# Optimization experiments

Measured on AMD Instinct MI355X. Metric: run time of the kernel, lower is better.

Reference implementation:

```python
import jax, jax.numpy as jnp
import numpy as np

D_MODEL = 512
KEY_DIM = 512
VALUE_DIM = 512
N_HEADS = 8


def setup_inputs() -> dict:
    key = jax.random.key(0)
    ks = jax.random.split(key, 12)
    B, S = 8, 1024
    s = 0.02
    return {
        "input1": jax.random.normal(ks[0], (B, S, D_MODEL), jnp.float32),
        "input2": jax.random.normal(ks[1], (B, S, D_MODEL), jnp.float32),
        "input3": jax.random.normal(ks[2], (B, S, D_MODEL), jnp.float32),
        # per-head projection weights stacked over heads: [H, D, d]
        "Wq": jax.random.normal(ks[3], (N_HEADS, D_MODEL, KEY_DIM), jnp.float32) * s,
        "bq": jnp.zeros((N_HEADS, KEY_DIM), jnp.float32),
        "Wk": jax.random.normal(ks[4], (N_HEADS, D_MODEL, KEY_DIM), jnp.float32) * s,
        "bk": jnp.zeros((N_HEADS, KEY_DIM), jnp.float32),
        "Wv": jax.random.normal(ks[5], (N_HEADS, D_MODEL, VALUE_DIM), jnp.float32) * s,
        "bv": jnp.zeros((N_HEADS, VALUE_DIM), jnp.float32),
        # output projection: concat of heads (H*VALUE_DIM) -> KEY_DIM
        "Wo": jax.random.normal(ks[6], (N_HEADS * VALUE_DIM, KEY_DIM), jnp.float32) * s,
        "bo": jnp.zeros((KEY_DIM,), jnp.float32),
    }


def reference(input1, input2, input3, Wq, bq, Wk, bk, Wv, bv, Wo, bo):
    # Batched equivalent of the per-head Python loop:
    # each head: q=Dense_q(input1), k=Dense_k(input2), v=Dense_v(input3);
    # softmax(q k^T / sqrt(key_dim)) v; concat over heads; Dense w_o.
    q = jnp.einsum("bsd,hde->bhse", input1, Wq) + bq[None, :, None, :]
    k = jnp.einsum("bsd,hde->bhse", input2, Wk) + bk[None, :, None, :]
    v = jnp.einsum("bsd,hde->bhse", input3, Wv) + bv[None, :, None, :]
    scale = 1.0 / jnp.sqrt(jnp.asarray(KEY_DIM, q.dtype))
    scores = jnp.einsum("bhqe,bhke->bhqk", q, k) * scale  # [B,H,S,S]
    attn = jax.nn.softmax(scores, axis=-1)
    heads = jnp.einsum("bhqk,bhke->bhqe", attn, v)  # [B,H,S,VALUE_DIM]
    B, H, S, E = heads.shape
    concat = jnp.transpose(heads, (0, 2, 1, 3)).reshape(B, S, H * E)
    return concat @ Wo + bo
```

## Files before the change

kernel.cpp:

```cpp
#include <hip/hip_runtime.h>
#include <hip/hip_bf16.h>

#define DEV static __device__ __forceinline__

typedef float f32x4 __attribute__((ext_vector_type(4)));
typedef __bf16 b16x8 __attribute__((ext_vector_type(8)));

DEV unsigned short f2bf(float f) {
  union { __hip_bfloat16 h; unsigned short u; } cv;
  cv.h = __float2bfloat16(f);
  return cv.u;
}

DEV void gload_lds16(const unsigned short* g, unsigned short* l) {
  __builtin_amdgcn_global_load_lds(
      (__attribute__((address_space(1))) void*)g,
      (__attribute__((address_space(3))) void*)l, 16, 0, 0);
}

__global__ __launch_bounds__(256) void k_convall(
    const float* __restrict__ in1, const float* __restrict__ in2,
    const float* __restrict__ in3, const float* __restrict__ Wq,
    const float* __restrict__ Wk, const float* __restrict__ Wv,
    unsigned short* __restrict__ in1b, unsigned short* __restrict__ in2b,
    unsigned short* __restrict__ in3b, unsigned short* __restrict__ wqb,
    unsigned short* __restrict__ wkb, unsigned short* __restrict__ wvb) {
  const int b = blockIdx.x;
  const float* src;
  unsigned short* dst;
  long long off;
  if (b < 4096) { src = in1; dst = in1b; off = b; }
  else if (b < 8192) { src = in2; dst = in2b; off = b - 4096; }
  else if (b < 12288) { src = in3; dst = in3b; off = b - 8192; }
  else if (b < 14336) { src = Wq; dst = wqb; off = b - 12288; }
  else if (b < 16384) { src = Wk; dst = wkb; off = b - 14336; }
  else { src = Wv; dst = wvb; off = b - 16384; }
  const long long i = off * 256 + threadIdx.x;
  const float4 v = ((const float4*)src)[i];
  ushort4 o;
  o.x = f2bf(v.x); o.y = f2bf(v.y); o.z = f2bf(v.z); o.w = f2bf(v.w);
  ((ushort4*)dst)[i] = o;
}

__global__ __launch_bounds__(256) void k_transpose_bf16(const float* __restrict__ src,
                                                        unsigned short* __restrict__ dst,
                                                        int R, int C) {
  __shared__ float t[32][33];
  const long long zo = (long long)blockIdx.z * R * C;
  const int c0 = blockIdx.x * 32, r0 = blockIdx.y * 32;
  const int tx = threadIdx.x & 31, ty = threadIdx.x >> 5;
#pragma unroll
  for (int i = 0; i < 4; ++i)
    t[ty + i * 8][tx] = src[zo + (long long)(r0 + ty + i * 8) * C + c0 + tx];
  __syncthreads();
#pragma unroll
  for (int i = 0; i < 4; ++i)
    dst[zo + (long long)(c0 + ty + i * 8) * R + r0 + tx] = f2bf(t[tx][ty + i * 8]);
}

__global__ __launch_bounds__(256) void k_uv(const float* __restrict__ Wq, const float* __restrict__ bk,
                                            const float* __restrict__ Wk, const float* __restrict__ bq,
                                            float* __restrict__ u, float* __restrict__ v) {
  const int sel = blockIdx.y;
  const float* W = sel ? Wk : Wq;
  const float* bb = sel ? bq : bk;
  float* dst = sel ? v : u;
  const int wave = threadIdx.x >> 6, lane = threadIdx.x & 63;
  const int idx = blockIdx.x * 4 + wave;
  const int h = idx >> 9, d = idx & 511;
  const float* wr = W + ((long long)h * 512 + d) * 512 + lane * 8;
  const float* br = bb + h * 512 + lane * 8;
  float s = 0.f;
#pragma unroll
  for (int k = 0; k < 8; ++k) s += wr[k] * br[k];
#pragma unroll
  for (int off = 32; off; off >>= 1) s += __shfl_xor(s, off);
  if (lane == 0) dst[h * 512 + d] = s;
}

__global__ __launch_bounds__(512) void k_bdot(const float* __restrict__ bq,
                                              const float* __restrict__ bk,
                                              float* __restrict__ c) {
  const int wave = threadIdx.x >> 6, lane = threadIdx.x & 63;
  const float* a = bq + wave * 512 + lane * 8;
  const float* b = bk + wave * 512 + lane * 8;
  float s = 0.f;
#pragma unroll
  for (int k = 0; k < 8; ++k) s += a[k] * b[k];
#pragma unroll
  for (int off = 32; off; off >>= 1) s += __shfl_xor(s, off);
  if (lane == 0) c[wave] = s;
}

__global__ __launch_bounds__(256) void k_rtct(const float* __restrict__ in1, const float* __restrict__ in2,
                                              const float* __restrict__ u, const float* __restrict__ v,
                                              const float* __restrict__ cbuf,
                                              float* __restrict__ rt, float* __restrict__ ct) {
  const int sel = blockIdx.y;
  const float* src = sel ? in2 : in1;
  const float* vec = sel ? v : u;
  float* dst = sel ? ct : rt;
  const int row = blockIdx.x;
  __shared__ float x[512];
  const float* p = src + (long long)row * 512;
  x[threadIdx.x] = p[threadIdx.x];
  x[threadIdx.x + 256] = p[threadIdx.x + 256];
  __syncthreads();
  const int wave = threadIdx.x >> 6, lane = threadIdx.x & 63;
  const int b = row >> 10, i = row & 1023;
#pragma unroll
  for (int t = 0; t < 2; ++t) {
    const int h = wave * 2 + t;
    const float* wv = vec + h * 512;
    float s = 0.f;
#pragma unroll
    for (int k = 0; k < 8; ++k) s += x[lane + k * 64] * wv[lane + k * 64];
#pragma unroll
    for (int off = 32; off; off >>= 1) s += __shfl_xor(s, off);
    if (lane == 0)
      dst[((long long)(b * 8 + h)) * 1024 + i] = s + (sel ? 0.f : cbuf[h]);
  }
}

__global__ __launch_bounds__(256) void k_bvo(const float* __restrict__ Wo,
                                             const float* __restrict__ bv,
                                             float* __restrict__ bvo) {
  const int h = blockIdx.x;
  __shared__ float bs[512];
  bs[threadIdx.x] = bv[h * 512 + threadIdx.x];
  bs[threadIdx.x + 256] = bv[h * 512 + threadIdx.x + 256];
  __syncthreads();
  float a0 = 0.f, a1 = 0.f;
  for (int e = 0; e < 512; ++e) {
    const float* row = Wo + ((long long)(h * 512 + e)) * 512;
    a0 += bs[e] * row[threadIdx.x];
    a1 += bs[e] * row[threadIdx.x + 256];
  }
  bvo[h * 512 + threadIdx.x] = a0;
  bvo[h * 512 + threadIdx.x + 256] = a1;
}

__global__ __launch_bounds__(256) void k_softmax_bf16(unsigned short* __restrict__ P) {
  const int wave = threadIdx.x >> 6, lane = threadIdx.x & 63;
  unsigned short* p = P + ((long long)blockIdx.x * 4 + wave) * 1024 + lane * 16;
  const b16x8 v0 = *(const b16x8*)p;
  const b16x8 v1 = *(const b16x8*)(p + 8);
  float f[16];
#pragma unroll
  for (int j = 0; j < 8; ++j) { f[j] = (float)v0[j]; f[8 + j] = (float)v1[j]; }
  float mx = f[0];
#pragma unroll
  for (int j = 1; j < 16; ++j) mx = fmaxf(mx, f[j]);
#pragma unroll
  for (int off = 32; off; off >>= 1) mx = fmaxf(mx, __shfl_xor(mx, off));
  float sum = 0.f;
#pragma unroll
  for (int j = 0; j < 16; ++j) { f[j] = __expf(f[j] - mx); sum += f[j]; }
#pragma unroll
  for (int off = 32; off; off >>= 1) sum += __shfl_xor(sum, off);
  const float inv = 1.f / sum;
  b16x8 o0, o1;
#pragma unroll
  for (int j = 0; j < 8; ++j) { o0[j] = (__bf16)(f[j] * inv); o1[j] = (__bf16)(f[8 + j] * inv); }
  *(b16x8*)p = o0;
  *(b16x8*)(p + 8) = o1;
}

template <int OM>
__global__ __launch_bounds__(256) void k_gemm_bt(
    const unsigned short* __restrict__ A, const unsigned short* __restrict__ Bt,
    void* __restrict__ Cv, const float* __restrict__ bias,
    const float* __restrict__ rAdd, const float* __restrict__ cAdd,
    int K, int lda, int ldb, int ldc,
    int azs, int azm, long long azr,
    int bzs, int bzm, long long bzr,
    int czs, long long czr, int czm, int czc,
    int biasm, int bstr, int rstr, float scale) {
  __shared__ unsigned short lA[128 * 64];
  __shared__ unsigned short lB[128 * 64];
  const int tid = threadIdx.x, wave = tid >> 6, lane = tid & 63;
  const int z = blockIdx.z;
  const int m0 = blockIdx.y * 128, n0 = blockIdx.x * 128;
  const unsigned short* Az = A + (long long)((z >> azs) & azm) * azr + (long long)m0 * lda;
  const unsigned short* Bz = Bt + (long long)((z >> bzs) & bzm) * bzr + (long long)n0 * ldb;

  const int srow = wave * 32 + (lane >> 3);
  const int scol = (lane & 7) * 8;
  const unsigned short* ga = Az + (long long)srow * lda + scol;
  const unsigned short* gb = Bz + (long long)srow * ldb + scol;
  unsigned short* laBase = &lA[(wave * 32) * 64];
  unsigned short* lbBase = &lB[(wave * 32) * 64];

  f32x4 acc[4][4] = {};
  const int wr = (wave >> 1) * 64, wc = (wave & 1) * 64;
  const int fr = lane & 15, kq = (lane >> 4) * 8;

  for (int k0 = 0; k0 < K; k0 += 64) {
#pragma unroll
    for (int i = 0; i < 4; ++i) {
      gload_lds16(ga + (long long)(i * 8) * lda + k0, laBase + (i * 8) * 64);
      gload_lds16(gb + (long long)(i * 8) * ldb + k0, lbBase + (i * 8) * 64);
    }
    __syncthreads();
#pragma unroll
    for (int kk = 0; kk < 64; kk += 32) {
      b16x8 af[4], bf[4];
#pragma unroll
      for (int i = 0; i < 4; ++i)
        af[i] = *(const b16x8*)&lA[(wr + i * 16 + fr) * 64 + kk + kq];
#pragma unroll
      for (int j = 0; j < 4; ++j)
        bf[j] = *(const b16x8*)&lB[(wc + j * 16 + fr) * 64 + kk + kq];
#pragma unroll
      for (int i = 0; i < 4; ++i)
#pragma unroll
        for (int j = 0; j < 4; ++j)
          acc[i][j] = __builtin_amdgcn_mfma_f32_16x16x32_bf16(af[i], bf[j], acc[i][j], 0, 0, 0);
    }
    __syncthreads();
  }

  const long long coff = (long long)(z >> czs) * czr + (long long)(z & czm) * czc;
  const long long zr = (long long)z * rstr;
  const int rr = (lane >> 4) * 4;
#pragma unroll
  for (int j = 0; j < 4; ++j) {
    const int col = n0 + wc + j * 16 + fr;
    const float bval = bias ? bias[(long long)(z & biasm) * bstr + col] : 0.f;
    const float ca = cAdd ? cAdd[zr + col] : 0.f;
#pragma unroll
    for (int i = 0; i < 4; ++i) {
#pragma unroll
      for (int r = 0; r < 4; ++r) {
        const int row = m0 + wr + i * 16 + rr + r;
        const float ra = rAdd ? rAdd[zr + row] : 0.f;
        const float val = (acc[i][j][r] + ra + ca) * scale + bval;
        if constexpr (OM == 1) {
          ((unsigned short*)Cv)[coff + (long long)row * ldc + col] = f2bf(val);
        } else if constexpr (OM == 2) {
          ((unsigned short*)Cv)[coff + (long long)col * ldc + row] = f2bf(val);
        } else {
          ((float*)Cv)[coff + (long long)row * ldc + col] = val;
        }
      }
    }
  }
}

#define STAGE_A8(nb, koff, i)                                  \
  gload_lds16(gaL + (long long)((i) * 8) * lda + (koff) + scol, \
              &sh[nb][(wid * 32 + (i) * 8) * 64])
#define STAGE_B8(nb, koff, i)                                  \
  gload_lds16(gbL + (long long)((i) * 8) * ldb + (koff) + scol, \
              &sh[2 + (nb)][(wid * 32 + (i) * 8) * 64])

template <int OM>
__global__ __launch_bounds__(512, 2) void k_gemm8p(
    const unsigned short* __restrict__ A, const unsigned short* __restrict__ Bt,
    void* __restrict__ Cv, const float* __restrict__ bias,
    const float* __restrict__ rAdd, const float* __restrict__ cAdd,
    int K, int lda, int ldb, int ldc,
    int azs, int azm, long long azr,
    int bzs, int bzm, long long bzr,
    int czs, long long czr, int czm, int czc,
    int biasm, int bstr, int rstr, float scale, int kzm, int kzr) {
  __shared__ unsigned short sh[4][256 * 64];
  const int tid = threadIdx.x, wid = tid >> 6, lane = tid & 63;
  const int wm = wid >> 2, wn = wid & 3;

  const int gx = gridDim.x, gy = gridDim.y;
  const int nwg = gx * gy * gridDim.z;
  const int bidL = blockIdx.x + gx * (blockIdx.y + gy * blockIdx.z);
  const int q8 = nwg >> 3;
  const int idx = (bidL & 7) * q8 + (bidL >> 3);
  const int bx = idx % gx;
  const int rem = idx / gx;
  const int by = rem % gy;
  const int z = rem / gy;

  const int m0 = by * 256, n0 = bx * 256;
  const int kstart = (z & kzm) * kzr;
  const unsigned short* Az = A + (long long)((z >> azs) & azm) * azr + (long long)m0 * lda + kstart;
  const unsigned short* Bz = Bt + (long long)((z >> bzs) & bzm) * bzr + (long long)n0 * ldb + kstart;

  const int scol = (((lane & 7) ^ ((lane >> 3) & 7)) << 3);
  const unsigned short* gaL = Az + (long long)(wid * 32 + (lane >> 3)) * lda;
  const unsigned short* gbL = Bz + (long long)(wid * 32 + (lane >> 3)) * ldb;

  const int fr = lane & 15, kq = (lane >> 4) * 8;
  const int fsw = (fr & 7) << 3;
  const int rc0 = kq ^ fsw;
  const int rc1 = (32 + kq) ^ fsw;
  const int aBase = (wm * 128 + fr) * 64;
  const int bBase = (wn * 64 + fr) * 64;

  f32x4 acc[8][4] = {};
  b16x8 afr[4][2], bfr[4][2];
  const int NT = K >> 6;

#pragma unroll
  for (int i = 0; i < 4; ++i) { STAGE_A8(0, 0, i); STAGE_B8(0, 0, i); }

  for (int kt = 0; kt < NT; ++kt) {
    const int cur = kt & 1, nb = cur ^ 1;
    if (kt + 1 < NT) {
      const int ko = (kt + 1) << 6;
#pragma unroll
      for (int i = 0; i < 4; ++i) { STAGE_A8(nb, ko, i); STAGE_B8(nb, ko, i); }
      asm volatile("s_waitcnt vmcnt(8)" ::: "memory");
    } else {
      asm volatile("s_waitcnt vmcnt(0)" ::: "memory");
    }
    __builtin_amdgcn_s_barrier();
    __builtin_amdgcn_sched_barrier(0);

#pragma unroll
    for (int i = 0; i < 4; ++i) {
      afr[i][0] = *(const b16x8*)&sh[cur][aBase + i * 1024 + rc0];
      afr[i][1] = *(const b16x8*)&sh[cur][aBase + i * 1024 + rc1];
    }
#pragma unroll
    for (int j = 0; j < 2; ++j) {
      bfr[j][0] = *(const b16x8*)&sh[2 + cur][bBase + j * 1024 + rc0];
      bfr[j][1] = *(const b16x8*)&sh[2 + cur][bBase + j * 1024 + rc1];
    }
    __builtin_amdgcn_s_setprio(1);
#pragma unroll
    for (int t = 0; t < 2; ++t)
#pragma unroll
      for (int i = 0; i < 4; ++i)
#pragma unroll
        for (int j = 0; j < 2; ++j)
          acc[i][j] = __builtin_amdgcn_mfma_f32_16x16x32_bf16(afr[i][t], bfr[j][t], acc[i][j], 0, 0, 0);
    __builtin_amdgcn_s_setprio(0);
#pragma unroll
    for (int j = 2; j < 4; ++j) {
      bfr[j][0] = *(const b16x8*)&sh[2 + cur][bBase + j * 1024 + rc0];
      bfr[j][1] = *(const b16x8*)&sh[2 + cur][bBase + j * 1024 + rc1];
    }
    __builtin_amdgcn_s_setprio(1);
#pragma unroll
    for (int t = 0; t < 2; ++t)
#pragma unroll
      for (int i = 0; i < 4; ++i)
#pragma unroll
        for (int j = 2; j < 4; ++j)
          acc[i][j] = __builtin_amdgcn_mfma_f32_16x16x32_bf16(afr[i][t], bfr[j][t], acc[i][j], 0, 0, 0);
    __builtin_amdgcn_s_setprio(0);
#pragma unroll
    for (int i = 0; i < 4; ++i) {
      afr[i][0] = *(const b16x8*)&sh[cur][aBase + (i + 4) * 1024 + rc0];
      afr[i][1] = *(const b16x8*)&sh[cur][aBase + (i + 4) * 1024 + rc1];
    }
    __builtin_amdgcn_s_setprio(1);
#pragma unroll
    for (int t = 0; t < 2; ++t)
#pragma unroll
      for (int i = 0; i < 4; ++i)
#pragma unroll
        for (int j = 0; j < 2; ++j)
          acc[i + 4][j] = __builtin_amdgcn_mfma_f32_16x16x32_bf16(afr[i][t], bfr[j][t], acc[i + 4][j], 0, 0, 0);
    __builtin_amdgcn_s_setprio(0);
    __builtin_amdgcn_s_setprio(1);
#pragma unroll
    for (int t = 0; t < 2; ++t)
#pragma unroll
      for (int i = 0; i < 4; ++i)
#pragma unroll
        for (int j = 2; j < 4; ++j)
          acc[i + 4][j] = __builtin_amdgcn_mfma_f32_16x16x32_bf16(afr[i][t], bfr[j][t], acc[i + 4][j], 0, 0, 0);
    __builtin_amdgcn_s_setprio(0);

    __builtin_amdgcn_s_barrier();
  }

  const long long coff = (long long)(z >> czs) * czr + (long long)(z & czm) * czc;
  const long long zr = (long long)z * rstr;
  const int rr = (lane >> 4) * 4;
  unsigned short* flat = &sh[0][0];

#pragma unroll
  for (int j = 0; j < 4; ++j) {
    const int col = n0 + wn * 64 + j * 16 + fr;
    const float bval = bias ? bias[(long long)(z & biasm) * bstr + col] : 0.f;
    const float ca = cAdd ? cAdd[zr + col] : 0.f;
#pragma unroll
    for (int i = 0; i < 8; ++i) {
#pragma unroll
      for (int r = 0; r < 4; ++r) {
        const int row = m0 + wm * 128 + i * 16 + rr + r;
        const float ra = rAdd ? rAdd[zr + row] : 0.f;
        const float val = (acc[i][j][r] + ra + ca) * scale + bval;
        const int rowL = wm * 128 + i * 16 + rr + r;
        const int colL = wn * 64 + j * 16 + fr;
        const int sR = (OM == 2) ? colL : rowL;
        const int sC = (OM == 2) ? rowL : colL;
        flat[sR * 256 + (sC ^ ((sR & 7) << 3))] = f2bf(val);
      }
    }
  }
  __builtin_amdgcn_s_barrier();
  const long long rbase = (OM == 2) ? (long long)n0 : (long long)m0;
  const long long cbase = (OM == 2) ? (long long)m0 : (long long)n0;
  unsigned short* Cb = (unsigned short*)Cv;
#pragma unroll
  for (int it = 0; it < 16; ++it) {
    const int t = it * 512 + tid;
    const int R = t >> 5;
    const int Cq = t & 31;
    const int q = Cq ^ (R & 7);
    const b16x8 v = *(const b16x8*)&flat[R * 256 + q * 8];
    *(b16x8*)(Cb + coff + (rbase + R) * ldc + cbase + Cq * 8) = v;
  }
}

#define STAGE_GA(nb, koff, i)                                  \
  gload_lds16(gaL + (long long)((i) * 8) * lda + (koff) + scol, \
              &sh[nb][(wid * 32 + (i) * 8) * 64])
#define STAGE_GB(nb, koff, i)                                  \
  gload_lds16(gbL + (long long)((i) * 8) * ldb + (koff) + scol, \
              &sh[2 + (nb)][(wid * 32 + (i) * 8) * 64])

template <int OM>
__global__ __launch_bounds__(256, 2) void k_g128(
    const unsigned short* __restrict__ A, const unsigned short* __restrict__ Bt,
    void* __restrict__ Cv, const float* __restrict__ bias,
    const float* __restrict__ rAdd, const float* __restrict__ cAdd,
    int K, int lda, int ldb, int ldc,
    int azs, int azm, long long azr,
    int bzs, int bzm, long long bzr,
    int czs, long long czr, int czm, int czc,
    int biasm, int bstr, int rstr, float scale, int kzm, int kzr) {
  __shared__ unsigned short sh[4][128 * 64];
  const int tid = threadIdx.x, wid = tid >> 6, lane = tid & 63;
  const int wm = wid >> 1, wn = wid & 1;

  const int gx = gridDim.x, gy = gridDim.y;
  const int nwg = gx * gy * gridDim.z;
  const int bidL = blockIdx.x + gx * (blockIdx.y + gy * blockIdx.z);
  const int q8 = nwg >> 3;
  const int idx = (bidL & 7) * q8 + (bidL >> 3);
  const int bx = idx % gx;
  const int rem = idx / gx;
  const int by = rem % gy;
  const int z = rem / gy;

  const int m0 = by * 128, n0 = bx * 128;
  const int kstart = (z & kzm) * kzr;
  const unsigned short* Az = A + (long long)((z >> azs) & azm) * azr + (long long)m0 * lda + kstart;
  const unsigned short* Bz = Bt + (long long)((z >> bzs) & bzm) * bzr + (long long)n0 * ldb + kstart;

  const int scol = (((lane & 7) ^ ((lane >> 3) & 7)) << 3);
  const unsigned short* gaL = Az + (long long)(wid * 32 + (lane >> 3)) * lda;
  const unsigned short* gbL = Bz + (long long)(wid * 32 + (lane >> 3)) * ldb;

  const int fr = lane & 15, kq = (lane >> 4) * 8;
  const int fsw = (fr & 7) << 3;
  const int rc0 = kq ^ fsw;
  const int rc1 = (32 + kq) ^ fsw;
  const int aBase = (wm * 64 + fr) * 64;
  const int bBase = (wn * 64 + fr) * 64;

  f32x4 acc[4][4] = {};
  b16x8 afr[4][2], bfr[4][2];
  const int NT = K >> 6;

#pragma unroll
  for (int i = 0; i < 4; ++i) { STAGE_GA(0, 0, i); STAGE_GB(0, 0, i); }

  for (int kt = 0; kt < NT; ++kt) {
    const int cur = kt & 1, nb = cur ^ 1;
    if (kt + 1 < NT) {
      const int ko = (kt + 1) << 6;
#pragma unroll
      for (int i = 0; i < 4; ++i) { STAGE_GA(nb, ko, i); STAGE_GB(nb, ko, i); }
      asm volatile("s_waitcnt vmcnt(8)" ::: "memory");
    } else {
      asm volatile("s_waitcnt vmcnt(0)" ::: "memory");
    }
    __builtin_amdgcn_s_barrier();
    __builtin_amdgcn_sched_barrier(0);

#pragma unroll
    for (int i = 0; i < 4; ++i) {
      afr[i][0] = *(const b16x8*)&sh[cur][aBase + i * 1024 + rc0];
      afr[i][1] = *(const b16x8*)&sh[cur][aBase + i * 1024 + rc1];
    }
#pragma unroll
    for (int j = 0; j < 4; ++j) {
      bfr[j][0] = *(const b16x8*)&sh[2 + cur][bBase + j * 1024 + rc0];
      bfr[j][1] = *(const b16x8*)&sh[2 + cur][bBase + j * 1024 + rc1];
    }
#pragma unroll
    for (int t = 0; t < 2; ++t)
#pragma unroll
      for (int i = 0; i < 4; ++i)
#pragma unroll
        for (int j = 0; j < 4; ++j)
          acc[i][j] = __builtin_amdgcn_mfma_f32_16x16x32_bf16(afr[i][t], bfr[j][t], acc[i][j], 0, 0, 0);

    __builtin_amdgcn_s_barrier();
  }

  const long long coff = (long long)(z >> czs) * czr + (long long)(z & czm) * czc;
  const long long zr = (long long)z * rstr;
  const int rr = (lane >> 4) * 4;
  unsigned short* flat = &sh[0][0];

  if constexpr (OM == 1 || OM == 2) {
#pragma unroll
    for (int j = 0; j < 4; ++j) {
      const int col = n0 + wn * 64 + j * 16 + fr;
      const float bval = bias ? bias[(long long)(z & biasm) * bstr + col] : 0.f;
      const float ca = cAdd ? cAdd[zr + col] : 0.f;
#pragma unroll
      for (int i = 0; i < 4; ++i) {
#pragma unroll
        for (int r = 0; r < 4; ++r) {
          const int row = m0 + wm * 64 + i * 16 + rr + r;
          const float ra = rAdd ? rAdd[zr + row] : 0.f;
          const float val = (acc[i][j][r] + ra + ca) * scale + bval;
          const int rowL = wm * 64 + i * 16 + rr + r;
          const int colL = wn * 64 + j * 16 + fr;
          const int sR = (OM == 2) ? colL : rowL;
          const int sC = (OM == 2) ? rowL : colL;
          flat[sR * 128 + (sC ^ ((sR & 7) << 3))] = f2bf(val);
        }
      }
    }
    __builtin_amdgcn_s_barrier();
    const long long rbase = (OM == 2) ? (long long)n0 : (long long)m0;
    const long long cbase = (OM == 2) ? (long long)m0 : (long long)n0;
    unsigned short* Cb = (unsigned short*)Cv;
#pragma unroll
    for (int it = 0; it < 8; ++it) {
      const int t = it * 256 + tid;
      const int R = t >> 4;
      const int Cq = t & 15;
      const int q = Cq ^ (R & 7);
      const b16x8 v = *(const b16x8*)&flat[R * 128 + q * 8];
      *(b16x8*)(Cb + coff + (rbase + R) * ldc + cbase + Cq * 8) = v;
    }
  } else {
    float* fflat = (float*)flat;
    float* Cf = (float*)Cv;
#pragma unroll
    for (int j = 0; j < 4; ++j) {
      const int col = n0 + wn * 64 + j * 16 + fr;
      const float bval = bias ? bias[(long long)(z & biasm) * bstr + col] : 0.f;
      const float ca = cAdd ? cAdd[zr + col] : 0.f;
#pragma unroll
      for (int i = 0; i < 4; ++i) {
#pragma unroll
        for (int r = 0; r < 4; ++r) {
          const int row = m0 + wm * 64 + i * 16 + rr + r;
          const float ra = rAdd ? rAdd[zr + row] : 0.f;
          const float val = (acc[i][j][r] + ra + ca) * scale + bval;
          const int Rl = wm * 64 + i * 16 + rr + r;
          const int Cl = wn * 64 + j * 16 + fr;
          fflat[Rl * 128 + (Cl ^ ((Rl & 7) << 2))] = val;
        }
      }
    }
    __builtin_amdgcn_s_barrier();
#pragma unroll
    for (int it = 0; it < 16; ++it) {
      const int t = it * 256 + tid;
      const int R = t >> 5;
      const int Cq = t & 31;
      const int q = Cq ^ (R & 7);
      const float4 v = *(const float4*)&fflat[R * 128 + q * 4];
      *(float4*)(Cf + coff + (long long)(m0 + R) * ldc + n0 + Cq * 4) = v;
    }
  }
}

extern "C" void kernel_launch(void* const* d_in, const int* in_sizes, int n_in,
                              void* d_out, int out_size, void* d_ws, size_t ws_size,
                              hipStream_t stream) {
  const float* in1 = (const float*)d_in[0];
  const float* in2 = (const float*)d_in[1];
  const float* in3 = (const float*)d_in[2];
  const float* Wq = (const float*)d_in[3];
  const float* bq = (const float*)d_in[4];
  const float* Wk = (const float*)d_in[5];
  const float* bk = (const float*)d_in[6];
  const float* Wv = (const float*)d_in[7];
  const float* bv = (const float*)d_in[8];
  const float* Wo = (const float*)d_in[9];
  const float* bo = (const float*)d_in[10];

  const long long MB = 1024 * 1024;
  typedef unsigned short us;
  unsigned char* w = (unsigned char*)d_ws;
  us* in2b = (us*)(w);
  us* Tbuf = (us*)(w + 8 * MB);
  us* Ubuf = (us*)(w + 8 * MB);
  us* Pcat = (us*)(w + 72 * MB);
  us* in1b = (us*)(w + 200 * MB);
  us* in3b = (us*)(w + 208 * MB);
  us* wqb = (us*)(w + 216 * MB);
  us* Wvot = (us*)(w + 216 * MB);
  us* wkb = (us*)(w + 220 * MB);
  us* wvb = (us*)(w + 224 * MB);
  us* wotb = (us*)(w + 228 * MB);
  us* Gt = (us*)(w + 232 * MB);
  float* rt = (float*)(w + 236 * MB);
  float* ct = (float*)(w + 236 * MB + (256 << 10));
  float* ubuf = (float*)(w + 237 * MB);
  float* vbuf = (float*)(w + 237 * MB + (16 << 10));
  float* cbuf = (float*)(w + 237 * MB + (32 << 10));
  float* bvo = (float*)(w + 237 * MB + (48 << 10));
  if ((long long)ws_size < 238 * MB) return;

  const float iscale = 0.04419417382415922f;
  const long long SD = 1024 * 512;

  k_convall<<<18432, 256, 0, stream>>>(in1, in2, in3, Wq, Wk, Wv,
                                       in1b, in2b, in3b, wqb, wkb, wvb);
  k_transpose_bf16<<<dim3(16, 128, 1), 256, 0, stream>>>(Wo, wotb, 4096, 512);

  k_uv<<<dim3(1024, 2), 256, 0, stream>>>(Wq, bk, Wk, bq, ubuf, vbuf);
  k_bdot<<<1, 512, 0, stream>>>(bq, bk, cbuf);
  k_rtct<<<dim3(8192, 2), 256, 0, stream>>>(in1, in2, ubuf, vbuf, cbuf, rt, ct);

  k_gemm_bt<1><<<dim3(4, 4, 8), 256, 0, stream>>>(
      wkb, wqb, Gt, nullptr, nullptr, nullptr, 512, 512, 512, 512,
      0, 7, 262144LL, 0, 7, 262144LL, 0, 262144LL, 0, 0, 0, 0, 0, 1.f);

  k_gemm_bt<1><<<dim3(4, 4, 8), 256, 0, stream>>>(
      wotb, wvb, Wvot, nullptr, nullptr, nullptr, 512, 4096, 512, 512,
      0, 7, 512LL, 0, 7, 262144LL, 0, 262144LL, 0, 0, 0, 0, 0, 1.f);
  k_bvo<<<8, 256, 0, stream>>>(Wo, bv, bvo);

  k_gemm8p<1><<<dim3(2, 4, 64), 512, 0, stream>>>(
      in1b, Gt, Tbuf, nullptr, nullptr, nullptr, 512, 512, 512, 512,
      3, 7, SD, 0, 7, 262144LL, 0, SD, 0, 0, 0, 0, 0, 1.f, 0, 0);

  k_gemm8p<1><<<dim3(4, 4, 64), 512, 0, stream>>>(
      Tbuf, in2b, Pcat, nullptr, rt, ct, 512, 512, 512, 8192,
      0, 63, SD, 3, 7, SD, 3, 8388608LL, 7, 1024, 0, 0, 1024, iscale, 0, 0);

  k_softmax_bf16<<<16384, 256, 0, stream>>>(Pcat);

  k_gemm8p<2><<<dim3(2, 4, 64), 512, 0, stream>>>(
      in3b, Wvot, Ubuf, bvo, nullptr, nullptr, 512, 512, 512, 8192,
      3, 7, SD, 0, 7, 262144LL, 3, 4194304LL, 7, 1024, 7, 512, 0, 1.f, 0, 0);

  k_g128<0><<<dim3(4, 8, 8), 256, 0, stream>>>(
      Pcat, Ubuf, d_out, bo, nullptr, nullptr, 8192, 8192, 8192, 512,
      0, 7, 8388608LL, 0, 7, 4194304LL, 0, 524288LL, 0, 0, 0, 0, 0, 1.f, 0, 0);
}
```

Baseline: 452.8 us.

## Fuse softmax exp into score GEMM and defer normalization to output GEMM

Removes the standalone softmax kernel. The score GEMM epilogue now applies exp to each value and accumulates per-row, per-head sums with atomics into a zeroed buffer. The final output GEMM accumulates each head's 512-wide K segment separately and scales it by the reciprocal row sum before adding it to the total. This saves one full read-write pass over the large bf16 probability matrix. In exchange it drops max subtraction, so it relies on scores staying small enough not to overflow, and it adds atomics, a memset and extra accumulator registers.

```diff
diff --git a/kernel.cpp b/kernel.cpp
--- a/kernel.cpp
+++ b/kernel.cpp
@@ -140,32 +140,6 @@
   bvo[h * 512 + threadIdx.x + 256] = a1;
 }
 
-__global__ __launch_bounds__(256) void k_softmax_bf16(unsigned short* __restrict__ P) {
-  const int wave = threadIdx.x >> 6, lane = threadIdx.x & 63;
-  unsigned short* p = P + ((long long)blockIdx.x * 4 + wave) * 1024 + lane * 16;
-  const b16x8 v0 = *(const b16x8*)p;
-  const b16x8 v1 = *(const b16x8*)(p + 8);
-  float f[16];
-#pragma unroll
-  for (int j = 0; j < 8; ++j) { f[j] = (float)v0[j]; f[8 + j] = (float)v1[j]; }
-  float mx = f[0];
-#pragma unroll
-  for (int j = 1; j < 16; ++j) mx = fmaxf(mx, f[j]);
-#pragma unroll
-  for (int off = 32; off; off >>= 1) mx = fmaxf(mx, __shfl_xor(mx, off));
-  float sum = 0.f;
-#pragma unroll
-  for (int j = 0; j < 16; ++j) { f[j] = __expf(f[j] - mx); sum += f[j]; }
-#pragma unroll
-  for (int off = 32; off; off >>= 1) sum += __shfl_xor(sum, off);
-  const float inv = 1.f / sum;
-  b16x8 o0, o1;
-#pragma unroll
-  for (int j = 0; j < 8; ++j) { o0[j] = (__bf16)(f[j] * inv); o1[j] = (__bf16)(f[8 + j] * inv); }
-  *(b16x8*)p = o0;
-  *(b16x8*)(p + 8) = o1;
-}
-
 template <int OM>
 __global__ __launch_bounds__(256) void k_gemm_bt(
     const unsigned short* __restrict__ A, const unsigned short* __restrict__ Bt,
@@ -254,11 +228,12 @@
   gload_lds16(gbL + (long long)((i) * 8) * ldb + (koff) + scol, \
               &sh[2 + (nb)][(wid * 32 + (i) * 8) * 64])
 
-template <int OM>
+template <int OM, int ES>
 __global__ __launch_bounds__(512, 2) void k_gemm8p(
     const unsigned short* __restrict__ A, const unsigned short* __restrict__ Bt,
     void* __restrict__ Cv, const float* __restrict__ bias,
     const float* __restrict__ rAdd, const float* __restrict__ cAdd,
+    float* __restrict__ rsum,
     int K, int lda, int ldb, int ldc,
     int azs, int azm, long long azr,
     int bzs, int bzm, long long bzr,
@@ -379,6 +354,14 @@
   const int rr = (lane >> 4) * 4;
   unsigned short* flat = &sh[0][0];
 
+  float rp[8][4];
+  if constexpr (ES) {
+#pragma unroll
+    for (int i = 0; i < 8; ++i)
+#pragma unroll
+      for (int r = 0; r < 4; ++r) rp[i][r] = 0.f;
+  }
+
 #pragma unroll
   for (int j = 0; j < 4; ++j) {
     const int col = n0 + wn * 64 + j * 16 + fr;
@@ -390,7 +373,11 @@
       for (int r = 0; r < 4; ++r) {
         const int row = m0 + wm * 128 + i * 16 + rr + r;
         const float ra = rAdd ? rAdd[zr + row] : 0.f;
-        const float val = (acc[i][j][r] + ra + ca) * scale + bval;
+        float val = (acc[i][j][r] + ra + ca) * scale + bval;
+        if constexpr (ES) {
+          val = __expf(val);
+          rp[i][r] += val;
+        }
         const int rowL = wm * 128 + i * 16 + rr + r;
         const int colL = wn * 64 + j * 16 + fr;
         const int sR = (OM == 2) ? colL : rowL;
@@ -398,6 +385,22 @@
         flat[sR * 256 + (sC ^ ((sR & 7) << 3))] = f2bf(val);
       }
     }
+  }
+  if constexpr (ES) {
+#pragma unroll
+    for (int i = 0; i < 8; ++i)
+#pragma unroll
+      for (int r = 0; r < 4; ++r) {
+        float v = rp[i][r];
+        v += __shfl_xor(v, 1); v += __shfl_xor(v, 2);
+        v += __shfl_xor(v, 4); v += __shfl_xor(v, 8);
+        if (fr == 0) {
+          const int rowL = wm * 128 + i * 16 + rr + r;
+          const long long ridx =
+              ((long long)(z >> 3) * 1024 + m0 + rowL) * 8 + (z & 7);
+          atomicAdd(&rsum[ridx], v);
+        }
+      }
   }
   __builtin_amdgcn_s_barrier();
   const long long rbase = (OM == 2) ? (long long)n0 : (long long)m0;
@@ -421,17 +424,18 @@
   gload_lds16(gbL + (long long)((i) * 8) * ldb + (koff) + scol, \
               &sh[2 + (nb)][(wid * 32 + (i) * 8) * 64])
 
-template <int OM>
+template <int OM, int SEG>
 __global__ __launch_bounds__(256, 2) void k_g128(
     const unsigned short* __restrict__ A, const unsigned short* __restrict__ Bt,
     void* __restrict__ Cv, const float* __restrict__ bias,
-    const float* __restrict__ rAdd, const float* __restrict__ cAdd,
+    const float* __restrict__ rsum,
     int K, int lda, int ldb, int ldc,
     int azs, int azm, long long azr,
     int bzs, int bzm, long long bzr,
     int czs, long long czr, int czm, int czc,
-    int biasm, int bstr, int rstr, float scale, int kzm, int kzr) {
+    int biasm, int bstr, float scale, int kzm, int kzr) {
   __shared__ unsigned short sh[4][128 * 64];
+  __shared__ float rsl[1024];
   const int tid = threadIdx.x, wid = tid >> 6, lane = tid & 63;
   const int wm = wid >> 1, wn = wid & 1;
 
@@ -460,8 +464,19 @@
   const int rc1 = (32 + kq) ^ fsw;
   const int aBase = (wm * 64 + fr) * 64;
   const int bBase = (wn * 64 + fr) * 64;
+  const int rr = (lane >> 4) * 4;
+
+  if constexpr (SEG) {
+#pragma unroll
+    for (int qq = 0; qq < 4; ++qq) {
+      const int tt = tid * 4 + qq;
+      const int row = tt >> 3, hh = tt & 7;
+      rsl[tt] = 1.0f / rsum[((long long)z * 1024 + m0 + row) * 8 + hh];
+    }
+  }
 
   f32x4 acc[4][4] = {};
+  f32x4 accH[4][4] = {};
   b16x8 afr[4][2], bfr[4][2];
   const int NT = K >> 6;
 
@@ -496,15 +511,37 @@
 #pragma unroll
       for (int i = 0; i < 4; ++i)
 #pragma unroll
-        for (int j = 0; j < 4; ++j)
-          acc[i][j] = __builtin_amdgcn_mfma_f32_16x16x32_bf16(afr[i][t], bfr[j][t], acc[i][j], 0, 0, 0);
+        for (int j = 0; j < 4; ++j) {
+          if constexpr (SEG)
+            accH[i][j] = __builtin_amdgcn_mfma_f32_16x16x32_bf16(afr[i][t], bfr[j][t], accH[i][j], 0, 0, 0);
+          else
+            acc[i][j] = __builtin_amdgcn_mfma_f32_16x16x32_bf16(afr[i][t], bfr[j][t], acc[i][j], 0, 0, 0);
+        }
+
+    if constexpr (SEG) {
+      if ((kt & 15) == 15) {
+        const int hh = kt >> 4;
+#pragma unroll
+        for (int i = 0; i < 4; ++i) {
+          float sv[4];
+#pragma unroll
+          for (int r = 0; r < 4; ++r)
+            sv[r] = rsl[(wm * 64 + i * 16 + rr + r) * 8 + hh];
+#pragma unroll
+          for (int j = 0; j < 4; ++j)
+#pragma unroll
+            for (int r = 0; r < 4; ++r) {
+              acc[i][j][r] += accH[i][j][r] * sv[r];
+              accH[i][j][r] = 0.f;
+            }
+        }
+      }
+    }
 
     __builtin_amdgcn_s_barrier();
   }
 
   const long long coff = (long long)(z >> czs) * czr + (long long)(z & czm) * czc;
-  const long long zr = (long long)z * rstr;
-  const int rr = (lane >> 4) * 4;
   unsigned short* flat = &sh[0][0];
 
   if constexpr (OM == 1 || OM == 2) {
@@ -512,14 +549,11 @@
     for (int j = 0; j < 4; ++j) {
       const int col = n0 + wn * 64 + j * 16 + fr;
       const float bval = bias ? bias[(long long)(z & biasm) * bstr + col] : 0.f;
-      const float ca = cAdd ? cAdd[zr + col] : 0.f;
 #pragma unroll
       for (int i = 0; i < 4; ++i) {
 #pragma unroll
         for (int r = 0; r < 4; ++r) {
-          const int row = m0 + wm * 64 + i * 16 + rr + r;
-          const float ra = rAdd ? rAdd[zr + row] : 0.f;
-          const float val = (acc[i][j][r] + ra + ca) * scale + bval;
+          const float val = acc[i][j][r] * scale + bval;
           const int rowL = wm * 64 + i * 16 + rr + r;
           const int colL = wn * 64 + j * 16 + fr;
           const int sR = (OM == 2) ? colL : rowL;
@@ -548,14 +582,11 @@
     for (int j = 0; j < 4; ++j) {
       const int col = n0 + wn * 64 + j * 16 + fr;
       const float bval = bias ? bias[(long long)(z & biasm) * bstr + col] : 0.f;
-      const float ca = cAdd ? cAdd[zr + col] : 0.f;
 #pragma unroll
       for (int i = 0; i < 4; ++i) {
 #pragma unroll
         for (int r = 0; r < 4; ++r) {
-          const int row = m0 + wm * 64 + i * 16 + rr + r;
-          const float ra = rAdd ? rAdd[zr + row] : 0.f;
-          const float val = (acc[i][j][r] + ra + ca) * scale + bval;
+          const float val = acc[i][j][r] * scale + bval;
           const int Rl = wm * 64 + i * 16 + rr + r;
           const int Cl = wn * 64 + j * 16 + fr;
           fflat[Rl * 128 + (Cl ^ ((Rl & 7) << 2))] = val;
@@ -598,7 +629,7 @@
   us* Ubuf = (us*)(w + 8 * MB);
   us* Pcat = (us*)(w + 72 * MB);
   us* in1b = (us*)(w + 200 * MB);
-  us* in3b = (us*)(w + 208 * MB);
+  float* rsum = (float*)(w + 200 * MB);
   us* wqb = (us*)(w + 216 * MB);
   us* Wvot = (us*)(w + 216 * MB);
   us* wkb = (us*)(w + 220 * MB);
@@ -617,7 +648,8 @@
   const long long SD = 1024 * 512;
 
   k_convall<<<18432, 256, 0, stream>>>(in1, in2, in3, Wq, Wk, Wv,
-                                       in1b, in2b, in3b, wqb, wkb, wvb);
+                                       in1b, in2b, (us*)(w + 208 * MB), wqb, wkb, wvb);
+  us* in3b = (us*)(w + 208 * MB);
   k_transpose_bf16<<<dim3(16, 128, 1), 256, 0, stream>>>(Wo, wotb, 4096, 512);
 
   k_uv<<<dim3(1024, 2), 256, 0, stream>>>(Wq, bk, Wk, bq, ubuf, vbuf);
@@ -633,21 +665,21 @@
       0, 7, 512LL, 0, 7, 262144LL, 0, 262144LL, 0, 0, 0, 0, 0, 1.f);
   k_bvo<<<8, 256, 0, stream>>>(Wo, bv, bvo);
 
-  k_gemm8p<1><<<dim3(2, 4, 64), 512, 0, stream>>>(
-      in1b, Gt, Tbuf, nullptr, nullptr, nullptr, 512, 512, 512, 512,
+  k_gemm8p<1, 0><<<dim3(2, 4, 64), 512, 0, stream>>>(
+      in1b, Gt, Tbuf, nullptr, nullptr, nullptr, nullptr, 512, 512, 512, 512,
       3, 7, SD, 0, 7, 262144LL, 0, SD, 0, 0, 0, 0, 0, 1.f, 0, 0);
 
-  k_gemm8p<1><<<dim3(4, 4, 64), 512, 0, stream>>>(
-      Tbuf, in2b, Pcat, nullptr, rt, ct, 512, 512, 512, 8192,
+  hipMemsetAsync(rsum, 0, 2 * MB, stream);
+
+  k_gemm8p<1, 1><<<dim3(4, 4, 64), 512, 0, stream>>>(
+      Tbuf, in2b, Pcat, nullptr, rt, ct, rsum, 512, 512, 512, 8192,
       0, 63, SD, 3, 7, SD, 3, 8388608LL, 7, 1024, 0, 0, 1024, iscale, 0, 0);
 
-  k_softmax_bf16<<<16384, 256, 0, stream>>>(Pcat);
-
-  k_gemm8p<2><<<dim3(2, 4, 64), 512, 0, stream>>>(
-      in3b, Wvot, Ubuf, bvo, nullptr, nullptr, 512, 512, 512, 8192,
+  k_gemm8p<2, 0><<<dim3(2, 4, 64), 512, 0, stream>>>(
+      in3b, Wvot, Ubuf, bvo, nullptr, nullptr, nullptr, 512, 512, 512, 8192,
       3, 7, SD, 0, 7, 262144LL, 3, 4194304LL, 7, 1024, 7, 512, 0, 1.f, 0, 0);
 
-  k_g128<0><<<dim3(4, 8, 8), 256, 0, stream>>>(
-      Pcat, Ubuf, d_out, bo, nullptr, nullptr, 8192, 8192, 8192, 512,
-      0, 7, 8388608LL, 0, 7, 4194304LL, 0, 524288LL, 0, 0, 0, 0, 0, 1.f, 0, 0);
-}
+  k_g128<0, 1><<<dim3(4, 8, 8), 256, 0, stream>>>(
+      Pcat, Ubuf, d_out, bo, rsum, 8192, 8192, 8192, 512,
+      0, 7, 8388608LL, 0, 7, 4194304LL, 0, 524288LL, 0, 0, 0, 0, 1.f, 0, 0);
+}
```

New measurement: 560.9 us. 23.9% more time.
